# Performance work log

Hardware: AMD Instinct MI355X
Metric: run time of the kernel (lower is better)

Reference implementation:

```python
import jax, jax.numpy as jnp
import numpy as np

N_USERS, N_ITEMS, D, L = 100000, 30000, 64, 2
N = N_USERS + N_ITEMS
NNZ_ADJ, NNZ_SYM, NNZ_HERB = 4000000, 1600000, 480000


def spmm(rows, cols, vals, x, n):
    # sparse [n, m] @ dense [m, d] via gather + segment_sum
    return jax.ops.segment_sum(vals[:, None] * x[cols], rows, num_segments=n)


def setup_inputs():
    key = jax.random.key(0)
    ks = jax.random.split(key, 19)
    s = np.float32(1.0 / np.sqrt(D))  # xavier-like scale, keeps tanh unsaturated
    return {
        'user_embedding': jax.random.normal(ks[0], (N_USERS, D), jnp.float32) * s,
        'item_embedding': jax.random.normal(ks[1], (N_ITEMS, D), jnp.float32) * s,
        'adj_vals': jax.random.uniform(ks[2], (NNZ_ADJ,), jnp.float32),
        'sym_vals': jax.random.uniform(ks[3], (NNZ_SYM,), jnp.float32),
        'herb_vals': jax.random.uniform(ks[4], (NNZ_HERB,), jnp.float32),
        'Q_user': jax.random.normal(ks[5], (L, D, D), jnp.float32) * s,
        'Q_item': jax.random.normal(ks[6], (L, D, D), jnp.float32) * s,
        'W_gc_user': jax.random.normal(ks[7], (L, 2 * D, D), jnp.float32) * s,
        'W_gc_item': jax.random.normal(ks[8], (L, 2 * D, D), jnp.float32) * s,
        'b_gc_user': jax.random.normal(ks[9], (L, D), jnp.float32) * s,
        'b_gc_item': jax.random.normal(ks[10], (L, D), jnp.float32) * s,
        'M_user': jax.random.normal(ks[11], (D, D), jnp.float32) * s,
        'M_item': jax.random.normal(ks[12], (D, D), jnp.float32) * s,
        'adj_rows': jax.random.randint(ks[13], (NNZ_ADJ,), 0, N, jnp.int32),
        'adj_cols': jax.random.randint(ks[14], (NNZ_ADJ,), 0, N, jnp.int32),
        'sym_rows': jax.random.randint(ks[15], (NNZ_SYM,), 0, N_USERS, jnp.int32),
        'sym_cols': jax.random.randint(ks[16], (NNZ_SYM,), 0, N_USERS, jnp.int32),
        'herb_rows': jax.random.randint(ks[17], (NNZ_HERB,), 0, N_ITEMS, jnp.int32),
        'herb_cols': jax.random.randint(ks[18], (NNZ_HERB,), 0, N_ITEMS, jnp.int32),
    }


def reference(user_embedding, item_embedding, adj_vals, sym_vals, herb_vals,
              Q_user, Q_item, W_gc_user, W_gc_item, b_gc_user, b_gc_item,
              M_user, M_item, adj_rows, adj_cols, sym_rows, sym_cols,
              herb_rows, herb_cols):
    ego0 = jnp.concatenate([user_embedding, item_embedding], axis=0)  # [N, D]

    def graphsage_branch(Q, W, b):
        ego = ego0
        for k in range(L):  # loop over fixed small n_layers
            agg = spmm(adj_rows, adj_cols, adj_vals, ego, N)           # neighbor aggregate
            h = jnp.tanh(agg @ Q[k])                                    # Q transform
            ego = jnp.tanh(jnp.concatenate([ego, h], axis=1) @ W[k] + b[k])
            # mess_dropout = 0 -> identity (eval mode)
        nrm = jnp.sqrt(jnp.sum(ego * ego, axis=1, keepdims=True))
        return ego / jnp.maximum(nrm, 1e-12)                            # F.normalize(p=2, dim=1)

    u_all = graphsage_branch(Q_user, W_gc_user, b_gc_user)
    i_all = graphsage_branch(Q_item, W_gc_item, b_gc_item)
    u_g = u_all[:N_USERS]
    i_g = i_all[N_USERS:]

    user_pair = jnp.tanh(spmm(sym_rows, sym_cols, sym_vals, user_embedding, N_USERS) @ M_user)
    item_pair = jnp.tanh(spmm(herb_rows, herb_cols, herb_vals, item_embedding, N_ITEMS) @ M_item)

    # fusion == 'add'
    return jnp.concatenate([u_g + user_pair, i_g + item_pair], axis=0)  # [N, D]
```

## Files before the change

### kernel.cpp

```cpp
#include <hip/hip_runtime.h>
#include <hip/hip_fp16.h>

#define NU 100000
#define NI 30000
#define NT 130000
#define D  64
#define NNZ_ADJ  4000000
#define NNZ_SYM  1600000
#define NNZ_HERB 480000

#define CHUNK 4096
#define BROWS 512

#define NBLK_ADJ  977
#define NBLK_SYM  391
#define NBLK_HERB 118

#define NBUCK_ADJ  254
#define NBUCK_SYM  196
#define NBUCK_HERB 59
#define CAP_ADJ  17000
#define CAP_SYM  9500
#define CAP_HERB 9500

#define OFF_QU0 0
#define OFF_QI0 4096
#define OFF_QU1 8192
#define OFF_QI1 12288
#define OFF_WU0 16384
#define OFF_WI0 24576
#define OFF_WU1 32768
#define OFF_WI1 40960
#define OFF_MU  49152
#define OFF_MI  53248
#define WT_ELEMS 57344

typedef _Float16 f16x8 __attribute__((ext_vector_type(8)));
typedef float f32x4 __attribute__((ext_vector_type(4)));

__device__ inline f32x4 mfma_16x16x32(f16x8 a, f16x8 b, f32x4 c) {
  return __builtin_amdgcn_mfma_f32_16x16x32_f16(a, b, c, 0, 0, 0);
}
__device__ inline f16x8 ld8h(const __half* p) { return *(const f16x8*)p; }

__global__ __launch_bounds__(512) void binA_all(
    const int* __restrict__ r0, const int* __restrict__ c0,
    const float* __restrict__ v0, uint2* __restrict__ st0, int* __restrict__ bc0,
    const int* __restrict__ r1, const int* __restrict__ c1,
    const float* __restrict__ v1, uint2* __restrict__ st1, int* __restrict__ bc1,
    const int* __restrict__ r2, const int* __restrict__ c2,
    const float* __restrict__ v2, uint2* __restrict__ st2, int* __restrict__ bc2) {
  __shared__ int cnt[256], lexc[256], cur[256], gbase[256], wt[4];
  __shared__ uint2 lpk[CHUNK];
  int blk = blockIdx.x;
  const int* rows; const int* cols; const float* vals;
  uint2* staging; int* bcnt; int nnz, cap, base;
  if (blk < NBLK_ADJ) {
    rows = r0; cols = c0; vals = v0; staging = st0; bcnt = bc0;
    nnz = NNZ_ADJ; cap = CAP_ADJ; base = blk * CHUNK;
  } else if (blk < NBLK_ADJ + NBLK_SYM) {
    rows = r1; cols = c1; vals = v1; staging = st1; bcnt = bc1;
    nnz = NNZ_SYM; cap = CAP_SYM; base = (blk - NBLK_ADJ) * CHUNK;
  } else {
    rows = r2; cols = c2; vals = v2; staging = st2; bcnt = bc2;
    nnz = NNZ_HERB; cap = CAP_HERB; base = (blk - NBLK_ADJ - NBLK_SYM) * CHUNK;
  }
  int tid = threadIdx.x;
  int lim = min(CHUNK, nnz - base);
  if (tid < 256) cnt[tid] = 0;
  __syncthreads();
  for (int j = tid; j < lim; j += 512) {
    int r = rows[base + j];
    atomicAdd(&cnt[r >> 9], 1);
  }
  __syncthreads();
  int v = 0, s = 0;
  if (tid < 256) {
    int lane = tid & 63, w = tid >> 6;
    v = cnt[tid];
    s = v;
#pragma unroll
    for (int o = 1; o < 64; o <<= 1) {
      int t = __shfl_up(s, o, 64);
      if (lane >= o) s += t;
    }
    if (lane == 63) wt[w] = s;
  }
  __syncthreads();
  if (tid < 256) {
    int w = tid >> 6;
    int woff = 0;
    for (int j = 0; j < w; ++j) woff += wt[j];
    int exc = woff + s - v;
    lexc[tid] = exc;
    cur[tid] = exc;
    gbase[tid] = (v > 0) ? atomicAdd(&bcnt[tid], v) : 0;
  }
  __syncthreads();
  for (int j = tid; j < lim; j += 512) {
    int r = rows[base + j];
    int b = r >> 9;
    unsigned short hv = __half_as_ushort(__float2half(vals[base + j])) & 0x7fffu;
    unsigned cv = ((unsigned)cols[base + j] << 15) | hv;
    int pos = atomicAdd(&cur[b], 1);
    lpk[pos] = make_uint2((unsigned)r, cv);
  }
  __syncthreads();
  for (int i = tid; i < lim; i += 512) {
    uint2 e = lpk[i];
    int b = (int)(e.x >> 9);
    int d = gbase[b] + (i - lexc[b]);
    if (d < cap) staging[(size_t)b * cap + d] = e;
  }
}

__global__ __launch_bounds__(256) void bucket_scan3(
    int* __restrict__ bc, int* __restrict__ bb,
    int* __restrict__ ptr0, int* __restrict__ ptr1, int* __restrict__ ptr2) {
  __shared__ int wt[4];
  int g = blockIdx.x;
  const int* bcnt = bc + g * 256;
  int* bbase = bb + g * 256;
  int nbuck = g == 0 ? NBUCK_ADJ : g == 1 ? NBUCK_SYM : NBUCK_HERB;
  int n = g == 0 ? NT : g == 1 ? NU : NI;
  int* ptr = g == 0 ? ptr0 : g == 1 ? ptr1 : ptr2;
  int tid = threadIdx.x, lane = tid & 63, w = tid >> 6;
  int v = (tid < nbuck) ? bcnt[tid] : 0;
  int s = v;
#pragma unroll
  for (int o = 1; o < 64; o <<= 1) {
    int t = __shfl_up(s, o, 64);
    if (lane >= o) s += t;
  }
  if (lane == 63) wt[w] = s;
  __syncthreads();
  int woff = 0;
  for (int j = 0; j < w; ++j) woff += wt[j];
  if (tid < nbuck) bbase[tid] = woff + s - v;
  if (tid == 0) ptr[n] = wt[0] + wt[1] + wt[2] + wt[3];
}

__global__ __launch_bounds__(256) void binB_all(
    const uint2* __restrict__ st0, const int* __restrict__ bc0,
    const int* __restrict__ bb0, unsigned* __restrict__ pk0, int* __restrict__ ptr0,
    const uint2* __restrict__ st1, const int* __restrict__ bc1,
    const int* __restrict__ bb1, unsigned* __restrict__ pk1, int* __restrict__ ptr1,
    const uint2* __restrict__ st2, const int* __restrict__ bc2,
    const int* __restrict__ bb2, unsigned* __restrict__ pk2, int* __restrict__ ptr2) {
  __shared__ int rof[512];
  __shared__ int wt[4];
  int blk = blockIdx.x, tid = threadIdx.x;
  const uint2* staging; const int* bcnt; const int* bbase;
  unsigned* pk; int* ptr; int n, cap, b;
  if (blk < NBUCK_ADJ) {
    staging = st0; bcnt = bc0; bbase = bb0; pk = pk0; ptr = ptr0;
    n = NT; cap = CAP_ADJ; b = blk;
  } else if (blk < NBUCK_ADJ + NBUCK_SYM) {
    staging = st1; bcnt = bc1; bbase = bb1; pk = pk1; ptr = ptr1;
    n = NU; cap = CAP_SYM; b = blk - NBUCK_ADJ;
  } else {
    staging = st2; bcnt = bc2; bbase = bb2; pk = pk2; ptr = ptr2;
    n = NI; cap = CAP_HERB; b = blk - NBUCK_ADJ - NBUCK_SYM;
  }
  int cntb = min(bcnt[b], cap);
  int gb = bbase[b];
  const uint2* st = staging + (size_t)b * cap;
  for (int i = tid; i < 512; i += 256) rof[i] = 0;
  __syncthreads();
  for (int i = tid; i < cntb; i += 256) atomicAdd(&rof[st[i].x & 511], 1);
  __syncthreads();
  int v0 = rof[2 * tid], v1 = rof[2 * tid + 1], pv = v0 + v1;
  int lane = tid & 63, w = tid >> 6, s = pv;
#pragma unroll
  for (int o = 1; o < 64; o <<= 1) {
    int t = __shfl_up(s, o, 64);
    if (lane >= o) s += t;
  }
  if (lane == 63) wt[w] = s;
  __syncthreads();
  int woff = 0;
  for (int j = 0; j < w; ++j) woff += wt[j];
  int exc = woff + s - pv;
  int r0 = b * BROWS + 2 * tid;
  if (r0 < n) ptr[r0] = gb + exc;
  if (r0 + 1 < n) ptr[r0 + 1] = gb + exc + v0;
  rof[2 * tid] = exc;
  rof[2 * tid + 1] = exc + v0;
  __syncthreads();
  for (int i = tid; i < cntb; i += 256) {
    uint2 e = st[i];
    int pos = atomicAdd(&rof[e.x & 511], 1);
    pk[gb + pos] = e.y;
  }
}

__global__ __launch_bounds__(256) void to_half(
    const float* __restrict__ U, const float* __restrict__ I,
    __half* __restrict__ EH) {
  int idx = blockIdx.x * 256 + threadIdx.x;
  const int ub = NU * D / 4;
  float4 v = idx < ub ? ((const float4*)U)[idx] : ((const float4*)I)[idx - ub];
  __half2* dst = (__half2*)EH + (size_t)idx * 2;
  dst[0] = __floats2half2_rn(v.x, v.y);
  dst[1] = __floats2half2_rn(v.z, v.w);
}

__global__ __launch_bounds__(256) void prep_weights(
    const float* __restrict__ Qu, const float* __restrict__ Qi,
    const float* __restrict__ Wu, const float* __restrict__ Wi,
    const float* __restrict__ Mu, const float* __restrict__ Mi,
    __half* __restrict__ WT) {
  int gid = blockIdx.x * 256 + threadIdx.x;
  if (gid >= WT_ELEMS) return;
  const float* src;
  int e, K, base;
  if (gid < 16384) {
    int m = gid >> 12; e = gid & 4095; K = 64; base = m * 4096;
    src = (m == 0) ? Qu : (m == 1) ? Qi : (m == 2) ? Qu + 4096 : Qi + 4096;
  } else if (gid < 49152) {
    int t = gid - 16384;
    int m = t >> 13; e = t & 8191; K = 128; base = 16384 + m * 8192;
    src = (m == 0) ? Wu : (m == 1) ? Wi : (m == 2) ? Wu + 8192 : Wi + 8192;
  } else {
    int t = gid - 49152;
    int m = t >> 12; e = t & 4095; K = 64; base = 49152 + m * 4096;
    src = (m == 0) ? Mu : Mi;
  }
  int k = e >> 6, c = e & 63;
  WT[base + c * K + k] = __float2half(src[(size_t)k * 64 + c]);
}

#define EDGE16(p)                                                        \
  {                                                                      \
    uint2 xq_ = Xp[(size_t)((p) >> 15) << fshift];                       \
    float vf_ = __half2float(__ushort_as_half(                           \
        (unsigned short)((p) & 0x7fffu)));                               \
    __half2 x0_ = *(__half2*)&xq_.x, x1_ = *(__half2*)&xq_.y;            \
    a0 += vf_ * __half2float(__low2half(x0_));                           \
    a1 += vf_ * __half2float(__high2half(x0_));                          \
    a2 += vf_ * __half2float(__low2half(x1_));                           \
    a3 += vf_ * __half2float(__high2half(x1_));                          \
  }

#define SPMM16_LOOP()                                                    \
  float a0 = 0.f, a1 = 0.f, a2 = 0.f, a3 = 0.f;                          \
  int i = s;                                                             \
  for (; i + 3 < e; i += 4) {                                            \
    unsigned e0_ = pk[i], e1_ = pk[i + 1], e2_ = pk[i + 2], e3_ = pk[i + 3]; \
    EDGE16(e0_) EDGE16(e1_) EDGE16(e2_) EDGE16(e3_)                      \
  }                                                                      \
  for (; i < e; ++i) { unsigned eq_ = pk[i]; EDGE16(eq_) }

__global__ __launch_bounds__(256) void spmm16_agg0(
    const int* __restrict__ ptr, const unsigned* __restrict__ pk,
    const __half* __restrict__ EH, __half* __restrict__ AGG0h) {
  int vid = (blockIdx.x * 256 + threadIdx.x) >> 6;
  int lane = threadIdx.x & 63;
  int grp = lane >> 4, l16 = lane & 15;
  int r = vid * 4 + grp;
  if (r >= NT) return;
  const uint2* Xp = (const uint2*)EH + l16;
  const int fshift = 4;
  int s = ptr[r], e = ptr[r + 1];
  SPMM16_LOOP()
  __half2 o0 = __floats2half2_rn(a0, a1), o1 = __floats2half2_rn(a2, a3);
  ((uint2*)AGG0h)[(size_t)r * 16 + l16] =
      make_uint2(*(unsigned*)&o0, *(unsigned*)&o1);
}

__global__ __launch_bounds__(256) void spmm16_fused(
    const int* __restrict__ ptr_adj, const unsigned* __restrict__ pk_adj,
    const int* __restrict__ ptr_sym, const unsigned* __restrict__ pk_sym,
    const int* __restrict__ ptr_herb, const unsigned* __restrict__ pk_herb,
    const __half* __restrict__ ECH, const __half* __restrict__ EH,
    __half* __restrict__ AGGh, __half* __restrict__ PAIR) {
  int vid = (blockIdx.x * 256 + threadIdx.x) >> 6;
  int lane = threadIdx.x & 63;
  int grp = lane >> 4, l16 = lane & 15;
  const int* ptrg; const unsigned* pk; const uint2* Xp; __half* Y;
  int fshift, r;
  if (vid < NT / 4) {
    int rr = vid * 4;
    ptrg = ptr_adj; pk = pk_adj; fshift = 5;
    Xp = (const uint2*)(ECH + (rr < NU ? 0 : 64)) + l16;
    Y = AGGh; r = rr + grp;
  } else if (vid < (NT + NU) / 4) {
    int rr = vid * 4 - NT;
    ptrg = ptr_sym; pk = pk_sym; fshift = 4;
    Xp = (const uint2*)EH + l16;
    Y = PAIR; r = rr + grp;
  } else {
    int rr = vid * 4 - NT - NU;
    ptrg = ptr_herb; pk = pk_herb; fshift = 4;
    Xp = (const uint2*)(EH + (size_t)NU * D) + l16;
    Y = PAIR + (size_t)NU * D; r = rr + grp;
  }
  int s = ptrg[r], e = ptrg[r + 1];
  SPMM16_LOOP()
  __half2 o0 = __floats2half2_rn(a0, a1), o1 = __floats2half2_rn(a2, a3);
  ((uint2*)Y)[(size_t)r * 16 + l16] =
      make_uint2(*(unsigned*)&o0, *(unsigned*)&o1);
}

__global__ __launch_bounds__(256) void l0_mfma(
    const __half* __restrict__ AGG0h, const __half* __restrict__ EH,
    __half* __restrict__ ECH, const __half* __restrict__ WT,
    const float* __restrict__ bu, const float* __restrict__ bi) {
  __shared__ __half Hs[2][16][72];
  int tid = threadIdx.x;
  int wave = tid >> 6, lane = tid & 63;
  int rl = lane & 15, kg = lane >> 4;
  int rb = blockIdx.x * 16;
  int colg = wave * 16 + rl;

  const __half* Xr = AGG0h + (size_t)(rb + rl) * D + kg * 8;
  f16x8 ax0 = ld8h(Xr), ax1 = ld8h(Xr + 32);
  const __half* qu = WT + OFF_QU0 + (size_t)colg * 64 + kg * 8;
  const __half* qi = WT + OFF_QI0 + (size_t)colg * 64 + kg * 8;
  f32x4 hu = {0.f, 0.f, 0.f, 0.f}, hi = {0.f, 0.f, 0.f, 0.f};
  hu = mfma_16x16x32(ax0, ld8h(qu), hu);
  hu = mfma_16x16x32(ax1, ld8h(qu + 32), hu);
  hi = mfma_16x16x32(ax0, ld8h(qi), hi);
  hi = mfma_16x16x32(ax1, ld8h(qi + 32), hi);
#pragma unroll
  for (int r = 0; r < 4; ++r) {
    int row = kg * 4 + r;
    Hs[0][row][colg] = __float2half(tanhf(hu[r]));
    Hs[1][row][colg] = __float2half(tanhf(hi[r]));
  }
  __syncthreads();

  const __half* Er = EH + (size_t)(rb + rl) * D + kg * 8;
  f16x8 ae0 = ld8h(Er), ae1 = ld8h(Er + 32);
  f16x8 au0 = *(const f16x8*)&Hs[0][rl][kg * 8];
  f16x8 au1 = *(const f16x8*)&Hs[0][rl][32 + kg * 8];
  f16x8 ai0 = *(const f16x8*)&Hs[1][rl][kg * 8];
  f16x8 ai1 = *(const f16x8*)&Hs[1][rl][32 + kg * 8];
  const __half* wu = WT + OFF_WU0 + (size_t)colg * 128 + kg * 8;
  const __half* wi = WT + OFF_WI0 + (size_t)colg * 128 + kg * 8;
  f32x4 su = {0.f, 0.f, 0.f, 0.f}, si = {0.f, 0.f, 0.f, 0.f};
  su = mfma_16x16x32(ae0, ld8h(wu), su);
  su = mfma_16x16x32(ae1, ld8h(wu + 32), su);
  su = mfma_16x16x32(au0, ld8h(wu + 64), su);
  su = mfma_16x16x32(au1, ld8h(wu + 96), su);
  si = mfma_16x16x32(ae0, ld8h(wi), si);
  si = mfma_16x16x32(ae1, ld8h(wi + 32), si);
  si = mfma_16x16x32(ai0, ld8h(wi + 64), si);
  si = mfma_16x16x32(ai1, ld8h(wi + 96), si);
  float bbu = bu[colg], bbi = bi[colg];
#pragma unroll
  for (int r = 0; r < 4; ++r) {
    size_t row = (size_t)(rb + kg * 4 + r);
    ECH[row * 128 + colg] = __float2half(tanhf(su[r] + bbu));
    ECH[row * 128 + 64 + colg] = __float2half(tanhf(si[r] + bbi));
  }
}

__global__ __launch_bounds__(256) void l1_mfma(
    const __half* __restrict__ AGGh, const __half* __restrict__ ECH,
    const __half* __restrict__ PAIR, const __half* __restrict__ WT,
    int qoff, int woff, int moff,
    const float* __restrict__ b1, float* __restrict__ out,
    int row_start, int ec_off) {
  __shared__ __half Hs[16][72];
  __shared__ float Ss[16][68], Ps[16][68];
  int tid = threadIdx.x;
  int wave = tid >> 6, lane = tid & 63;
  int rl = lane & 15, kg = lane >> 4;
  int rb = row_start + blockIdx.x * 16;
  int colg = wave * 16 + rl;

  const __half* Xr = AGGh + (size_t)(rb + rl) * D + kg * 8;
  f16x8 ax0 = ld8h(Xr), ax1 = ld8h(Xr + 32);
  const __half* q1 = WT + qoff + (size_t)colg * 64 + kg * 8;
  f32x4 h = {0.f, 0.f, 0.f, 0.f};
  h = mfma_16x16x32(ax0, ld8h(q1), h);
  h = mfma_16x16x32(ax1, ld8h(q1 + 32), h);
#pragma unroll
  for (int r = 0; r < 4; ++r) Hs[kg * 4 + r][colg] = __float2half(tanhf(h[r]));
  __syncthreads();

  const __half* Er = ECH + (size_t)(rb + rl) * 128 + ec_off + kg * 8;
  f16x8 ae0 = ld8h(Er), ae1 = ld8h(Er + 32);
  f16x8 ah0 = *(const f16x8*)&Hs[rl][kg * 8];
  f16x8 ah1 = *(const f16x8*)&Hs[rl][32 + kg * 8];
  const __half* Pr = PAIR + (size_t)(rb + rl) * D + kg * 8;
  f16x8 ap0 = ld8h(Pr), ap1 = ld8h(Pr + 32);
  const __half* w1 = WT + woff + (size_t)colg * 128 + kg * 8;
  const __half* mm = WT + moff + (size_t)colg * 64 + kg * 8;
  f32x4 s = {0.f, 0.f, 0.f, 0.f}, sp = {0.f, 0.f, 0.f, 0.f};
  s = mfma_16x16x32(ae0, ld8h(w1), s);
  s = mfma_16x16x32(ae1, ld8h(w1 + 32), s);
  s = mfma_16x16x32(ah0, ld8h(w1 + 64), s);
  s = mfma_16x16x32(ah1, ld8h(w1 + 96), s);
  sp = mfma_16x16x32(ap0, ld8h(mm), sp);
  sp = mfma_16x16x32(ap1, ld8h(mm + 32), sp);
  float bb = b1[colg];
#pragma unroll
  for (int r = 0; r < 4; ++r) {
    Ss[kg * 4 + r][colg] = tanhf(s[r] + bb);
    Ps[kg * 4 + r][colg] = tanhf(sp[r]);
  }
  __syncthreads();

  int lr = tid >> 4, q = tid & 15;
  float4 v = *(float4*)&Ss[lr][q * 4];
  float4 p = *(float4*)&Ps[lr][q * 4];
  float ss = v.x * v.x + v.y * v.y + v.z * v.z + v.w * v.w;
  ss += __shfl_xor(ss, 1, 16);
  ss += __shfl_xor(ss, 2, 16);
  ss += __shfl_xor(ss, 4, 16);
  ss += __shfl_xor(ss, 8, 16);
  float inv = 1.0f / fmaxf(sqrtf(ss), 1e-12f);
  *(float4*)&out[(size_t)(rb + lr) * D + q * 4] =
      make_float4(v.x * inv + p.x, v.y * inv + p.y,
                  v.z * inv + p.z, v.w * inv + p.w);
}

extern "C" void kernel_launch(void* const* d_in, const int* in_sizes, int n_in,
                              void* d_out, int out_size, void* d_ws, size_t ws_size,
                              hipStream_t stream) {
  const float* user_emb = (const float*)d_in[0];
  const float* item_emb = (const float*)d_in[1];
  const float* adj_vals = (const float*)d_in[2];
  const float* sym_vals = (const float*)d_in[3];
  const float* herb_vals = (const float*)d_in[4];
  const float* Q_user = (const float*)d_in[5];
  const float* Q_item = (const float*)d_in[6];
  const float* W_user = (const float*)d_in[7];
  const float* W_item = (const float*)d_in[8];
  const float* b_user = (const float*)d_in[9];
  const float* b_item = (const float*)d_in[10];
  const float* M_user = (const float*)d_in[11];
  const float* M_item = (const float*)d_in[12];
  const int* adj_rows = (const int*)d_in[13];
  const int* adj_cols = (const int*)d_in[14];
  const int* sym_rows = (const int*)d_in[15];
  const int* sym_cols = (const int*)d_in[16];
  const int* herb_rows = (const int*)d_in[17];
  const int* herb_cols = (const int*)d_in[18];

  float* out = (float*)d_out;

  char* w = (char*)d_ws;
  size_t off = 0;
  auto alloc = [&](size_t bytes) -> void* {
    off = (off + 255) & ~(size_t)255;
    void* p = w + off;
    off += bytes;
    return p;
  };
  __half* EH    = (__half*)alloc((size_t)NT * D * 2);
  __half* AGG0h = (__half*)alloc((size_t)NT * D * 2);
  __half* ECH   = (__half*)alloc((size_t)NT * 128 * 2);
  __half* AGGh  = (__half*)alloc((size_t)NT * D * 2);
  int* ptr_adj  = (int*)alloc((size_t)(NT + 1) * 4);
  unsigned* pk_adj = (unsigned*)alloc((size_t)NNZ_ADJ * 4);
  int* ptr_sym  = (int*)alloc((size_t)(NU + 1) * 4);
  unsigned* pk_sym = (unsigned*)alloc((size_t)NNZ_SYM * 4);
  int* ptr_herb = (int*)alloc((size_t)(NI + 1) * 4);
  unsigned* pk_herb = (unsigned*)alloc((size_t)NNZ_HERB * 4);
  int* bc = (int*)alloc(768 * 4);
  int* bb = (int*)alloc(768 * 4);
  __half* WT = (__half*)alloc((size_t)WT_ELEMS * 2);

  uint2* st_adj  = (uint2*)ECH;
  uint2* st_sym  = (uint2*)AGG0h;
  uint2* st_herb = (uint2*)EH;

  prep_weights<<<(WT_ELEMS + 255) / 256, 256, 0, stream>>>(
      Q_user, Q_item, W_user, W_item, M_user, M_item, WT);

  hipMemsetAsync(bc, 0, 768 * 4, stream);
  binA_all<<<NBLK_ADJ + NBLK_SYM + NBLK_HERB, 512, 0, stream>>>(
      adj_rows, adj_cols, adj_vals, st_adj, bc,
      sym_rows, sym_cols, sym_vals, st_sym, bc + 256,
      herb_rows, herb_cols, herb_vals, st_herb, bc + 512);
  bucket_scan3<<<3, 256, 0, stream>>>(bc, bb, ptr_adj, ptr_sym, ptr_herb);
  binB_all<<<NBUCK_ADJ + NBUCK_SYM + NBUCK_HERB, 256, 0, stream>>>(
      st_adj, bc, bb, pk_adj, ptr_adj,
      st_sym, bc + 256, bb + 256, pk_sym, ptr_sym,
      st_herb, bc + 512, bb + 512, pk_herb, ptr_herb);

  to_half<<<NT * D / 4 / 256, 256, 0, stream>>>(user_emb, item_emb, EH);

  spmm16_agg0<<<NT / 4 * 64 / 256, 256, 0, stream>>>(ptr_adj, pk_adj, EH, AGG0h);
  l0_mfma<<<NT / 16, 256, 0, stream>>>(AGG0h, EH, ECH, WT, b_user, b_item);

  spmm16_fused<<<(NT + NU + NI) / 4 * 64 / 256, 256, 0, stream>>>(
      ptr_adj, pk_adj, ptr_sym, pk_sym, ptr_herb, pk_herb,
      ECH, EH, AGGh, AGG0h);

  l1_mfma<<<NU / 16, 256, 0, stream>>>(
      AGGh, ECH, AGG0h, WT, OFF_QU1, OFF_WU1, OFF_MU, b_user + 64, out, 0, 0);
  l1_mfma<<<NI / 16, 256, 0, stream>>>(
      AGGh, ECH, AGG0h, WT, OFF_QI1, OFF_WI1, OFF_MI, b_item + 64, out, NU, 64);
}
```

Before: 413.4 us.

## Store layer-0 outputs in FP8 to halve layer-1 gather traffic

Layer-0 ego embeddings (ECH) are now stored as FP8 (e4m3 via hardware convert when available) instead of fp16, so the layer-1 adjacency SpMM gathers 4 bytes per lane per edge instead of 8. The SpMM inner loops are unrolled to 8 edges, the two l1_mfma launches are merged into one, and the staging buffers are reassigned to accommodate the smaller ECH buffer. The FP8 quantization reduces precision of tanh outputs, which risks exceeding accuracy tolerance, and the software fallback uses a different encoding.

```diff
diff --git a/kernel.cpp b/kernel.cpp
--- a/kernel.cpp
+++ b/kernel.cpp
@@ -37,11 +37,45 @@
 
 typedef _Float16 f16x8 __attribute__((ext_vector_type(8)));
 typedef float f32x4 __attribute__((ext_vector_type(4)));
+typedef float f32x2 __attribute__((ext_vector_type(2)));
 
 __device__ inline f32x4 mfma_16x16x32(f16x8 a, f16x8 b, f32x4 c) {
   return __builtin_amdgcn_mfma_f32_16x16x32_f16(a, b, c, 0, 0, 0);
 }
 __device__ inline f16x8 ld8h(const __half* p) { return *(const f16x8*)p; }
+
+#if defined(__has_builtin)
+#if __has_builtin(__builtin_amdgcn_cvt_pk_f32_fp8) && \
+    __has_builtin(__builtin_amdgcn_cvt_pk_fp8_f32)
+#define FP8_HW 1
+#endif
+#endif
+
+__device__ inline void fp8x4_to_f32x4(unsigned w, float* o) {
+#ifdef FP8_HW
+  f32x2 a = __builtin_amdgcn_cvt_pk_f32_fp8(w, false);
+  f32x2 b = __builtin_amdgcn_cvt_pk_f32_fp8(w, true);
+  o[0] = a.x; o[1] = a.y; o[2] = b.x; o[3] = b.y;
+#else
+#pragma unroll
+  for (int k = 0; k < 4; ++k) {
+    unsigned bb = (w >> (8 * k)) & 0xffu;
+    unsigned short hb =
+        (unsigned short)(((bb & 0x80u) << 8) | ((bb & 0x7fu) << 7));
+    o[k] = __half2float(__ushort_as_half(hb)) * 256.0f;
+  }
+#endif
+}
+
+__device__ inline unsigned char f_to_fp8(float f) {
+#ifdef FP8_HW
+  return (unsigned char)(__builtin_amdgcn_cvt_pk_fp8_f32(f, f, 0, false) & 0xffu);
+#else
+  unsigned short hb = __half_as_ushort(__float2half(f * 0.00390625f));
+  unsigned short r = (unsigned short)((hb & 0x7fffu) + 0x0040u);
+  return (unsigned char)(((r >> 7) & 0x7fu) | ((hb >> 8) & 0x80u));
+#endif
+}
 
 __global__ __launch_bounds__(512) void binA_all(
     const int* __restrict__ r0, const int* __restrict__ c0,
@@ -232,7 +266,7 @@
 
 #define EDGE16(p)                                                        \
   {                                                                      \
-    uint2 xq_ = Xp[(size_t)((p) >> 15) << fshift];                       \
+    uint2 xq_ = Xp[(size_t)((p) >> 15) << 4];                            \
     float vf_ = __half2float(__ushort_as_half(                           \
         (unsigned short)((p) & 0x7fffu)));                               \
     __half2 x0_ = *(__half2*)&xq_.x, x1_ = *(__half2*)&xq_.y;            \
@@ -242,14 +276,18 @@
     a3 += vf_ * __half2float(__high2half(x1_));                          \
   }
 
-#define SPMM16_LOOP()                                                    \
-  float a0 = 0.f, a1 = 0.f, a2 = 0.f, a3 = 0.f;                          \
-  int i = s;                                                             \
-  for (; i + 3 < e; i += 4) {                                            \
-    unsigned e0_ = pk[i], e1_ = pk[i + 1], e2_ = pk[i + 2], e3_ = pk[i + 3]; \
-    EDGE16(e0_) EDGE16(e1_) EDGE16(e2_) EDGE16(e3_)                      \
-  }                                                                      \
-  for (; i < e; ++i) { unsigned eq_ = pk[i]; EDGE16(eq_) }
+#define EDGE8(p)                                                         \
+  {                                                                      \
+    unsigned w8_ = *(const unsigned*)(X8 + ((size_t)((p) >> 15) << 7));  \
+    float vf_ = __half2float(__ushort_as_half(                           \
+        (unsigned short)((p) & 0x7fffu)));                               \
+    float xf_[4];                                                        \
+    fp8x4_to_f32x4(w8_, xf_);                                            \
+    a0 += vf_ * xf_[0];                                                  \
+    a1 += vf_ * xf_[1];                                                  \
+    a2 += vf_ * xf_[2];                                                  \
+    a3 += vf_ * xf_[3];                                                  \
+  }
 
 __global__ __launch_bounds__(256) void spmm16_agg0(
     const int* __restrict__ ptr, const unsigned* __restrict__ pk,
@@ -260,9 +298,18 @@
   int r = vid * 4 + grp;
   if (r >= NT) return;
   const uint2* Xp = (const uint2*)EH + l16;
-  const int fshift = 4;
   int s = ptr[r], e = ptr[r + 1];
-  SPMM16_LOOP()
+  float a0 = 0.f, a1 = 0.f, a2 = 0.f, a3 = 0.f;
+  int i = s;
+  for (; i + 7 < e; i += 8) {
+    unsigned e0_ = pk[i],     e1_ = pk[i + 1];
+    unsigned e2_ = pk[i + 2], e3_ = pk[i + 3];
+    unsigned e4_ = pk[i + 4], e5_ = pk[i + 5];
+    unsigned e6_ = pk[i + 6], e7_ = pk[i + 7];
+    EDGE16(e0_) EDGE16(e1_) EDGE16(e2_) EDGE16(e3_)
+    EDGE16(e4_) EDGE16(e5_) EDGE16(e6_) EDGE16(e7_)
+  }
+  for (; i < e; ++i) { unsigned eq_ = pk[i]; EDGE16(eq_) }
   __half2 o0 = __floats2half2_rn(a0, a1), o1 = __floats2half2_rn(a2, a3);
   ((uint2*)AGG0h)[(size_t)r * 16 + l16] =
       make_uint2(*(unsigned*)&o0, *(unsigned*)&o1);
@@ -272,39 +319,64 @@
     const int* __restrict__ ptr_adj, const unsigned* __restrict__ pk_adj,
     const int* __restrict__ ptr_sym, const unsigned* __restrict__ pk_sym,
     const int* __restrict__ ptr_herb, const unsigned* __restrict__ pk_herb,
-    const __half* __restrict__ ECH, const __half* __restrict__ EH,
+    const unsigned char* __restrict__ ECH8, const __half* __restrict__ EH,
     __half* __restrict__ AGGh, __half* __restrict__ PAIR) {
   int vid = (blockIdx.x * 256 + threadIdx.x) >> 6;
   int lane = threadIdx.x & 63;
   int grp = lane >> 4, l16 = lane & 15;
-  const int* ptrg; const unsigned* pk; const uint2* Xp; __half* Y;
-  int fshift, r;
   if (vid < NT / 4) {
-    int rr = vid * 4;
-    ptrg = ptr_adj; pk = pk_adj; fshift = 5;
-    Xp = (const uint2*)(ECH + (rr < NU ? 0 : 64)) + l16;
-    Y = AGGh; r = rr + grp;
-  } else if (vid < (NT + NU) / 4) {
-    int rr = vid * 4 - NT;
-    ptrg = ptr_sym; pk = pk_sym; fshift = 4;
-    Xp = (const uint2*)EH + l16;
-    Y = PAIR; r = rr + grp;
+    int r = vid * 4 + grp;
+    const unsigned char* X8 = ECH8 + (vid * 4 < NU ? 0 : 64) + l16 * 4;
+    int s = ptr_adj[r], e = ptr_adj[r + 1];
+    float a0 = 0.f, a1 = 0.f, a2 = 0.f, a3 = 0.f;
+    int i = s;
+    for (; i + 7 < e; i += 8) {
+      unsigned e0_ = pk_adj[i],     e1_ = pk_adj[i + 1];
+      unsigned e2_ = pk_adj[i + 2], e3_ = pk_adj[i + 3];
+      unsigned e4_ = pk_adj[i + 4], e5_ = pk_adj[i + 5];
+      unsigned e6_ = pk_adj[i + 6], e7_ = pk_adj[i + 7];
+      EDGE8(e0_) EDGE8(e1_) EDGE8(e2_) EDGE8(e3_)
+      EDGE8(e4_) EDGE8(e5_) EDGE8(e6_) EDGE8(e7_)
+    }
+    for (; i < e; ++i) { unsigned eq_ = pk_adj[i]; EDGE8(eq_) }
+    __half2 o0 = __floats2half2_rn(a0, a1), o1 = __floats2half2_rn(a2, a3);
+    ((uint2*)AGGh)[(size_t)r * 16 + l16] =
+        make_uint2(*(unsigned*)&o0, *(unsigned*)&o1);
   } else {
-    int rr = vid * 4 - NT - NU;
-    ptrg = ptr_herb; pk = pk_herb; fshift = 4;
-    Xp = (const uint2*)(EH + (size_t)NU * D) + l16;
-    Y = PAIR + (size_t)NU * D; r = rr + grp;
-  }
-  int s = ptrg[r], e = ptrg[r + 1];
-  SPMM16_LOOP()
-  __half2 o0 = __floats2half2_rn(a0, a1), o1 = __floats2half2_rn(a2, a3);
-  ((uint2*)Y)[(size_t)r * 16 + l16] =
-      make_uint2(*(unsigned*)&o0, *(unsigned*)&o1);
+    const int* ptrg; const unsigned* pk; const uint2* Xp; __half* Y;
+    int r;
+    if (vid < (NT + NU) / 4) {
+      r = vid * 4 - NT + grp;
+      ptrg = ptr_sym; pk = pk_sym;
+      Xp = (const uint2*)EH + l16;
+      Y = PAIR;
+    } else {
+      r = vid * 4 - NT - NU + grp;
+      ptrg = ptr_herb; pk = pk_herb;
+      Xp = (const uint2*)(EH + (size_t)NU * D) + l16;
+      Y = PAIR + (size_t)NU * D;
+    }
+    int s = ptrg[r], e = ptrg[r + 1];
+    float a0 = 0.f, a1 = 0.f, a2 = 0.f, a3 = 0.f;
+    int i = s;
+    for (; i + 7 < e; i += 8) {
+      unsigned e0_ = pk[i],     e1_ = pk[i + 1];
+      unsigned e2_ = pk[i + 2], e3_ = pk[i + 3];
+      unsigned e4_ = pk[i + 4], e5_ = pk[i + 5];
+      unsigned e6_ = pk[i + 6], e7_ = pk[i + 7];
+      EDGE16(e0_) EDGE16(e1_) EDGE16(e2_) EDGE16(e3_)
+      EDGE16(e4_) EDGE16(e5_) EDGE16(e6_) EDGE16(e7_)
+    }
+    for (; i < e; ++i) { unsigned eq_ = pk[i]; EDGE16(eq_) }
+    __half2 o0 = __floats2half2_rn(a0, a1), o1 = __floats2half2_rn(a2, a3);
+    ((uint2*)Y)[(size_t)r * 16 + l16] =
+        make_uint2(*(unsigned*)&o0, *(unsigned*)&o1);
+  }
 }
 
 __global__ __launch_bounds__(256) void l0_mfma(
     const __half* __restrict__ AGG0h, const __half* __restrict__ EH,
-    __half* __restrict__ ECH, const __half* __restrict__ WT,
+    unsigned char* __restrict__ ECH8, const __half* __restrict__ WT,
     const float* __restrict__ bu, const float* __restrict__ bi) {
   __shared__ __half Hs[2][16][72];
   int tid = threadIdx.x;
@@ -351,23 +423,28 @@
 #pragma unroll
   for (int r = 0; r < 4; ++r) {
     size_t row = (size_t)(rb + kg * 4 + r);
-    ECH[row * 128 + colg] = __float2half(tanhf(su[r] + bbu));
-    ECH[row * 128 + 64 + colg] = __float2half(tanhf(si[r] + bbi));
+    ECH8[row * 128 + colg] = f_to_fp8(tanhf(su[r] + bbu));
+    ECH8[row * 128 + 64 + colg] = f_to_fp8(tanhf(si[r] + bbi));
   }
 }
 
 __global__ __launch_bounds__(256) void l1_mfma(
-    const __half* __restrict__ AGGh, const __half* __restrict__ ECH,
+    const __half* __restrict__ AGGh, const unsigned char* __restrict__ ECH8,
     const __half* __restrict__ PAIR, const __half* __restrict__ WT,
-    int qoff, int woff, int moff,
-    const float* __restrict__ b1, float* __restrict__ out,
-    int row_start, int ec_off) {
+    const float* __restrict__ bu, const float* __restrict__ bi,
+    float* __restrict__ out) {
   __shared__ __half Hs[16][72];
   __shared__ float Ss[16][68], Ps[16][68];
   int tid = threadIdx.x;
   int wave = tid >> 6, lane = tid & 63;
   int rl = lane & 15, kg = lane >> 4;
-  int rb = row_start + blockIdx.x * 16;
+  int rb = blockIdx.x * 16;
+  bool user = rb < NU;
+  int qoff = user ? OFF_QU1 : OFF_QI1;
+  int woff = user ? OFF_WU1 : OFF_WI1;
+  int moff = user ? OFF_MU : OFF_MI;
+  const float* b1 = (user ? bu : bi) + 64;
+  int ec_off = user ? 0 : 64;
   int colg = wave * 16 + rl;
 
   const __half* Xr = AGGh + (size_t)(rb + rl) * D + kg * 8;
@@ -380,8 +457,22 @@
   for (int r = 0; r < 4; ++r) Hs[kg * 4 + r][colg] = __float2half(tanhf(h[r]));
   __syncthreads();
 
-  const __half* Er = ECH + (size_t)(rb + rl) * 128 + ec_off + kg * 8;
-  f16x8 ae0 = ld8h(Er), ae1 = ld8h(Er + 32);
+  const unsigned char* Er = ECH8 + (size_t)(rb + rl) * 128 + ec_off + kg * 8;
+  uint2 w0 = *(const uint2*)Er;
+  uint2 w1v = *(const uint2*)(Er + 32);
+  float f0[4], f1[4], f2[4], f3[4];
+  fp8x4_to_f32x4(w0.x, f0);
+  fp8x4_to_f32x4(w0.y, f1);
+  fp8x4_to_f32x4(w1v.x, f2);
+  fp8x4_to_f32x4(w1v.y, f3);
+  f16x8 ae0, ae1;
+#pragma unroll
+  for (int k = 0; k < 4; ++k) {
+    ae0[k] = (_Float16)f0[k];
+    ae0[4 + k] = (_Float16)f1[k];
+    ae1[k] = (_Float16)f2[k];
+    ae1[4 + k] = (_Float16)f3[k];
+  }
   f16x8 ah0 = *(const f16x8*)&Hs[rl][kg * 8];
   f16x8 ah1 = *(const f16x8*)&Hs[rl][32 + kg * 8];
   const __half* Pr = PAIR + (size_t)(rb + rl) * D + kg * 8;
@@ -452,7 +543,7 @@
   };
   __half* EH    = (__half*)alloc((size_t)NT * D * 2);
   __half* AGG0h = (__half*)alloc((size_t)NT * D * 2);
-  __half* ECH   = (__half*)alloc((size_t)NT * 128 * 2);
+  unsigned char* ECH8 = (unsigned char*)alloc((size_t)NT * 128);
   __half* AGGh  = (__half*)alloc((size_t)NT * D * 2);
   int* ptr_adj  = (int*)alloc((size_t)(NT + 1) * 4);
   unsigned* pk_adj = (unsigned*)alloc((size_t)NNZ_ADJ * 4);
@@ -463,10 +554,10 @@
   int* bc = (int*)alloc(768 * 4);
   int* bb = (int*)alloc(768 * 4);
   __half* WT = (__half*)alloc((size_t)WT_ELEMS * 2);
-
-  uint2* st_adj  = (uint2*)ECH;
-  uint2* st_sym  = (uint2*)AGG0h;
-  uint2* st_herb = (uint2*)EH;
+  uint2* st_herb = (uint2*)alloc((size_t)NBUCK_HERB * CAP_HERB * 8);
+
+  uint2* st_adj = (uint2*)EH;
+  uint2* st_sym = (uint2*)AGGh;
 
   prep_weights<<<(WT_ELEMS + 255) / 256, 256, 0, stream>>>(
       Q_user, Q_item, W_user, W_item, M_user, M_item, WT);
@@ -485,14 +576,12 @@
   to_half<<<NT * D / 4 / 256, 256, 0, stream>>>(user_emb, item_emb, EH);
 
   spmm16_agg0<<<NT / 4 * 64 / 256, 256, 0, stream>>>(ptr_adj, pk_adj, EH, AGG0h);
-  l0_mfma<<<NT / 16, 256, 0, stream>>>(AGG0h, EH, ECH, WT, b_user, b_item);
+  l0_mfma<<<NT / 16, 256, 0, stream>>>(AGG0h, EH, ECH8, WT, b_user, b_item);
 
   spmm16_fused<<<(NT + NU + NI) / 4 * 64 / 256, 256, 0, stream>>>(
       ptr_adj, pk_adj, ptr_sym, pk_sym, ptr_herb, pk_herb,
-      ECH, EH, AGGh, AGG0h);
-
-  l1_mfma<<<NU / 16, 256, 0, stream>>>(
-      AGGh, ECH, AGG0h, WT, OFF_QU1, OFF_WU1, OFF_MU, b_user + 64, out, 0, 0);
-  l1_mfma<<<NI / 16, 256, 0, stream>>>(
-      AGGh, ECH, AGG0h, WT, OFF_QI1, OFF_WI1, OFF_MI, b_item + 64, out, NU, 64);
-}
+      ECH8, EH, AGGh, AGG0h);
+
+  l1_mfma<<<(NU + NI) / 16, 256, 0, stream>>>(
+      AGGh, ECH8, AGG0h, WT, b_user, b_item, out);
+}
```

After: 410.1 us. Within noise of the previous version (-0.8%).
